# Performance work log

Hardware: AMD Instinct MI355X
Metric: run time of the kernel (lower is better)

## Reference

```python
import jax, jax.numpy as jnp
import numpy as np

THRESHOLD = 0.5
EPS = 1e-6

def setup_inputs() -> dict:
    key = jax.random.key(0)
    k1, k2, k3 = jax.random.split(key, 3)
    x = jax.random.normal(k1, (8192, 4096), dtype=jnp.float32)
    weight = jax.random.normal(k2, (16384, 4096), dtype=jnp.float32) * 0.02
    bias = jax.random.normal(k3, (16384,), dtype=jnp.float32) * 0.01
    return {"x": x, "weight": weight, "bias": bias}

def _quantize(weight):
    # abs-mean scale, ternarize to {-1,0,+1} with threshold, rescale
    scale = jnp.maximum(jnp.mean(jnp.abs(weight)), EPS)
    normalized = weight / scale
    ternary = jnp.sign(normalized) * (jnp.abs(normalized) > THRESHOLD).astype(weight.dtype)
    return ternary * scale

def reference(x, weight, bias):
    weight_q = _quantize(weight)
    # F.linear: x @ W^T + b
    return jnp.einsum('ti,oi->to', x, weight_q) + bias
```

## Files before the change

### kernel.cpp

```cpp
#include <hip/hip_runtime.h>
#include <hip/hip_bf16.h>

#define GLOBAL_AS __attribute__((address_space(1)))
#define LDS_AS    __attribute__((address_space(3)))

typedef __attribute__((ext_vector_type(8))) __bf16 bf16x8;
typedef __attribute__((ext_vector_type(4))) float  f32x4;

static constexpr int M = 8192;
static constexpr int N = 16384;
static constexpr int K = 4096;
static constexpr float W_EPS = 1e-6f;
#define INV_WCOUNT (1.0f / 67108864.0f)

__global__ void absum_kernel(const float4* __restrict__ w, float* __restrict__ out) {
  const int total = (N * K) / 4;
  int idx = blockIdx.x * blockDim.x + threadIdx.x;
  int stride = gridDim.x * blockDim.x;
  float s = 0.0f;
  for (int i = idx; i < total; i += stride) {
    float4 v = w[i];
    s += fabsf(v.x) + fabsf(v.y) + fabsf(v.z) + fabsf(v.w);
  }
  #pragma unroll
  for (int off = 32; off > 0; off >>= 1) s += __shfl_down(s, off, 64);
  __shared__ float red[4];
  const int lane = threadIdx.x & 63, wv = threadIdx.x >> 6;
  if (lane == 0) red[wv] = s;
  __syncthreads();
  if (threadIdx.x == 0) atomicAdd(out, red[0] + red[1] + red[2] + red[3]);
}

__global__ void quant_kernel(const float4* __restrict__ w, ushort4* __restrict__ wq,
                             const float* __restrict__ wsum) {
  const float s   = fmaxf(wsum[0] * INV_WCOUNT, W_EPS);
  const float thr = 0.5f * s;
  const int total = (N * K) / 4;
  int idx = blockIdx.x * blockDim.x + threadIdx.x;
  int stride = gridDim.x * blockDim.x;
  for (int i = idx; i < total; i += stride) {
    float4 v = w[i];
    ushort4 q;
    q.x = v.x > thr ? 0x3F80u : (v.x < -thr ? 0xBF80u : 0u);
    q.y = v.y > thr ? 0x3F80u : (v.y < -thr ? 0xBF80u : 0u);
    q.z = v.z > thr ? 0x3F80u : (v.z < -thr ? 0xBF80u : 0u);
    q.w = v.w > thr ? 0x3F80u : (v.w < -thr ? 0xBF80u : 0u);
    wq[i] = q;
  }
}

__device__ __forceinline__ unsigned short f2bf(float f) {
  unsigned int b = __float_as_uint(f);
  b += 0x7FFFu + ((b >> 16) & 1u);
  return (unsigned short)(b >> 16);
}

__global__ void castx_kernel(const float4* __restrict__ x, ushort4* __restrict__ xb) {
  const int total = (M * K) / 4;
  int idx = blockIdx.x * blockDim.x + threadIdx.x;
  int stride = gridDim.x * blockDim.x;
  for (int i = idx; i < total; i += stride) {
    float4 v = x[i];
    ushort4 q;
    q.x = f2bf(v.x); q.y = f2bf(v.y); q.z = f2bf(v.z); q.w = f2bf(v.w);
    xb[i] = q;
  }
}

#define STAGE(gp, ldsbase, tt, h) do {                                               \
    char* _l = (ldsbase) + ((tt) & 1) * 32768 + (h) * 16384 + wv * 1024;             \
    __builtin_amdgcn_global_load_lds((const GLOBAL_AS void*)(gp[h][0] + (size_t)(tt) * 64), \
                                     (LDS_AS void*)_l, 16, 0, 0);                    \
    __builtin_amdgcn_global_load_lds((const GLOBAL_AS void*)(gp[h][1] + (size_t)(tt) * 64), \
                                     (LDS_AS void*)(_l + 8192), 16, 0, 0);           \
  } while (0)

#define DSA(ih, bb) do {                                                             \
    _Pragma("unroll")                                                                \
    for (int i = 0; i < 4; ++i) {                                                    \
      Af[ih][i][0] = *(const bf16x8*)(paA0 + (bb) * 32768 + ((ih) * 64 + i * 16) * 128); \
      Af[ih][i][1] = *(const bf16x8*)(paA1 + (bb) * 32768 + ((ih) * 64 + i * 16) * 128); \
    }                                                                                \
  } while (0)

#define DSB(jh, bb) do {                                                             \
    _Pragma("unroll")                                                                \
    for (int j = 0; j < 2; ++j) {                                                    \
      Bf[jh][j][0] = *(const bf16x8*)(pbB0 + (bb) * 32768 + ((jh) * 32 + j * 16) * 128); \
      Bf[jh][j][1] = *(const bf16x8*)(pbB1 + (bb) * 32768 + ((jh) * 32 + j * 16) * 128); \
    }                                                                                \
  } while (0)

#define MFMAQ(ih, jh) do {                                                           \
    _Pragma("unroll")                                                                \
    for (int kk = 0; kk < 2; ++kk)                                                   \
      _Pragma("unroll")                                                              \
      for (int i = 0; i < 4; ++i)                                                    \
        _Pragma("unroll")                                                            \
        for (int j = 0; j < 2; ++j)                                                  \
          acc[(ih) * 4 + i][(jh) * 2 + j] = __builtin_amdgcn_mfma_f32_16x16x32_bf16( \
              Af[ih][i][kk], Bf[jh][j][kk], acc[(ih) * 4 + i][(jh) * 2 + j], 0, 0, 0); \
  } while (0)

__global__ __launch_bounds__(512, 2) void gemm_kernel(
    const __hip_bfloat16* __restrict__ A,
    const __hip_bfloat16* __restrict__ B,
    const float* __restrict__ bias,
    const float* __restrict__ wsum,
    float* __restrict__ out) {
  extern __shared__ char smem[];
  char* ldsA = smem;
  char* ldsB = smem + 65536;

  const int tid  = threadIdx.x;
  const int lane = tid & 63;
  const int wv   = tid >> 6;
  const int wm   = wv >> 2;
  const int wn   = wv & 3;
  const int tn   = blockIdx.x;
  const int tm   = blockIdx.y;

  const int srow = tid >> 3;
  const int sce  = ((((tid & 7) << 4) ^ ((srow & 7) << 4)) >> 1);
  const __hip_bfloat16* gA[2][2];
  const __hip_bfloat16* gB[2][2];
  #pragma unroll
  for (int h = 0; h < 2; ++h)
    #pragma unroll
    for (int c = 0; c < 2; ++c) {
      gA[h][c] = A + (size_t)(tm * 256 + h * 128 + c * 64 + srow) * K + sce;
      gB[h][c] = B + (size_t)(tn * 256 + h * 128 + c * 64 + srow) * K + sce;
    }

  const int arow = wm * 128 + (lane & 15);
  const int brow = wn * 64  + (lane & 15);
  const int xorv = (lane & 7) << 4;
  const int ac0  = (((lane >> 4) << 4) + 0)  ^ xorv;
  const int ac1  = (((lane >> 4) << 4) + 64) ^ xorv;
  const char* paA0 = ldsA + arow * 128 + ac0;
  const char* paA1 = ldsA + arow * 128 + ac1;
  const char* pbB0 = ldsB + brow * 128 + ac0;
  const char* pbB1 = ldsB + brow * 128 + ac1;

  const f32x4 zero = {0.f, 0.f, 0.f, 0.f};
  f32x4 acc[8][4];
  #pragma unroll
  for (int i = 0; i < 8; ++i)
    #pragma unroll
    for (int j = 0; j < 4; ++j) acc[i][j] = zero;

  bf16x8 Af[2][4][2];
  bf16x8 Bf[2][2][2];

  STAGE(gA, ldsA, 0, 0); STAGE(gA, ldsA, 0, 1);
  STAGE(gB, ldsB, 0, 0); STAGE(gB, ldsB, 0, 1);
  STAGE(gA, ldsA, 1, 0); STAGE(gA, ldsA, 1, 1);
  asm volatile("s_waitcnt vmcnt(4)" ::: "memory");
  __builtin_amdgcn_s_barrier();

  for (int t = 0; t < 64; ++t) {
    const int bb = t & 1;
    DSA(0, bb); DSB(0, bb);
    if (t + 1 < 64) STAGE(gB, ldsB, t + 1, 0);
    __builtin_amdgcn_s_barrier();
    asm volatile("s_waitcnt lgkmcnt(0)" ::: "memory");
    __builtin_amdgcn_sched_barrier(0);
    __builtin_amdgcn_s_setprio(1);
    MFMAQ(0, 0);
    __builtin_amdgcn_s_setprio(0);
    __builtin_amdgcn_s_barrier();
    DSA(1, bb);
    if (t + 1 < 64) STAGE(gB, ldsB, t + 1, 1);
    __builtin_amdgcn_s_barrier();
    asm volatile("s_waitcnt lgkmcnt(0)" ::: "memory");
    __builtin_amdgcn_sched_barrier(0);
    __builtin_amdgcn_s_setprio(1);
    MFMAQ(1, 0);
    __builtin_amdgcn_s_setprio(0);
    __builtin_amdgcn_s_barrier();
    DSB(1, bb);
    if (t + 2 < 64) STAGE(gA, ldsA, t + 2, 0);
    __builtin_amdgcn_s_barrier();
    asm volatile("s_waitcnt lgkmcnt(0)" ::: "memory");
    __builtin_amdgcn_sched_barrier(0);
    __builtin_amdgcn_s_setprio(1);
    MFMAQ(1, 1);
    __builtin_amdgcn_s_setprio(0);
    __builtin_amdgcn_s_barrier();
    if (t + 2 < 64) STAGE(gA, ldsA, t + 2, 1);
    __builtin_amdgcn_s_barrier();
    __builtin_amdgcn_s_setprio(1);
    MFMAQ(0, 1);
    __builtin_amdgcn_s_setprio(0);
    if (t < 62) asm volatile("s_waitcnt vmcnt(4)" ::: "memory");
    else        asm volatile("s_waitcnt vmcnt(0)" ::: "memory");
    __builtin_amdgcn_s_barrier();
  }

  const float s  = fmaxf(wsum[0] * INV_WCOUNT, W_EPS);
  const int   n0 = tn * 256 + wn * 64 + (lane & 15);
  const int   m0 = tm * 256 + wm * 128 + ((lane >> 4) << 2);
  float bj[4];
  #pragma unroll
  for (int j = 0; j < 4; ++j) bj[j] = bias[n0 + j * 16];
  #pragma unroll
  for (int i = 0; i < 8; ++i) {
    #pragma unroll
    for (int r = 0; r < 4; ++r) {
      float* orow = out + (size_t)(m0 + i * 16 + r) * N + n0;
      #pragma unroll
      for (int j = 0; j < 4; ++j)
        orow[j * 16] = acc[i][j][r] * s + bj[j];
    }
  }
}

extern "C" void kernel_launch(void* const* d_in, const int* in_sizes, int n_in,
                              void* d_out, int out_size, void* d_ws, size_t ws_size,
                              hipStream_t stream) {
  const float* x    = (const float*)d_in[0];
  const float* w    = (const float*)d_in[1];
  const float* bias = (const float*)d_in[2];
  float* out = (float*)d_out;

  char* ws = (char*)d_ws;
  float* wsum = (float*)ws;
  __hip_bfloat16* Wq = (__hip_bfloat16*)(ws + 256);
  __hip_bfloat16* Xb = (__hip_bfloat16*)(ws + 256 + (size_t)N * K * 2);

  static bool attr_set = false;
  if (!attr_set) {
    hipFuncSetAttribute((const void*)gemm_kernel,
                        hipFuncAttributeMaxDynamicSharedMemorySize, 131072);
    attr_set = true;
  }

  hipMemsetAsync(wsum, 0, sizeof(float), stream);
  absum_kernel<<<2048, 256, 0, stream>>>((const float4*)w, wsum);
  quant_kernel<<<8192, 256, 0, stream>>>((const float4*)w, (ushort4*)Wq, wsum);
  castx_kernel<<<4096, 256, 0, stream>>>((const float4*)x, (ushort4*)Xb);
  dim3 grid(N / 256, M / 256);
  gemm_kernel<<<grid, 512, 131072, stream>>>(Xb, Wq, bias, wsum, out);
}
```

Before: 1.602 ms.

## Fuse quant and cast prep kernels and deepen GEMM B-tile prefetch

Merges the weight ternarization and the x-to-bf16 cast into one launch that splits work by block index and writes 16-byte vectors, removing a kernel launch and widening stores. In the GEMM main loop, the B half-tile for step t+2 is now issued one phase earlier, the vmcnt wait is relaxed from 4 to 6, and the loop is unrolled by two with explicit tail iterations. The intent is to hide more global-to-LDS latency behind MFMA work, at the cost of tighter LDS buffer-reuse ordering that must stay correct across the barriers.

```diff
diff --git a/kernel.cpp b/kernel.cpp
--- a/kernel.cpp
+++ b/kernel.cpp
@@ -6,6 +6,7 @@
 
 typedef __attribute__((ext_vector_type(8))) __bf16 bf16x8;
 typedef __attribute__((ext_vector_type(4))) float  f32x4;
+typedef __attribute__((ext_vector_type(8))) unsigned short ushort8_t;
 
 static constexpr int M = 8192;
 static constexpr int N = 16384;
@@ -31,39 +32,44 @@
   if (threadIdx.x == 0) atomicAdd(out, red[0] + red[1] + red[2] + red[3]);
 }
 
-__global__ void quant_kernel(const float4* __restrict__ w, ushort4* __restrict__ wq,
-                             const float* __restrict__ wsum) {
-  const float s   = fmaxf(wsum[0] * INV_WCOUNT, W_EPS);
-  const float thr = 0.5f * s;
-  const int total = (N * K) / 4;
-  int idx = blockIdx.x * blockDim.x + threadIdx.x;
-  int stride = gridDim.x * blockDim.x;
-  for (int i = idx; i < total; i += stride) {
-    float4 v = w[i];
-    ushort4 q;
-    q.x = v.x > thr ? 0x3F80u : (v.x < -thr ? 0xBF80u : 0u);
-    q.y = v.y > thr ? 0x3F80u : (v.y < -thr ? 0xBF80u : 0u);
-    q.z = v.z > thr ? 0x3F80u : (v.z < -thr ? 0xBF80u : 0u);
-    q.w = v.w > thr ? 0x3F80u : (v.w < -thr ? 0xBF80u : 0u);
-    wq[i] = q;
-  }
-}
-
 __device__ __forceinline__ unsigned short f2bf(float f) {
   unsigned int b = __float_as_uint(f);
   b += 0x7FFFu + ((b >> 16) & 1u);
   return (unsigned short)(b >> 16);
 }
 
-__global__ void castx_kernel(const float4* __restrict__ x, ushort4* __restrict__ xb) {
-  const int total = (M * K) / 4;
-  int idx = blockIdx.x * blockDim.x + threadIdx.x;
-  int stride = gridDim.x * blockDim.x;
-  for (int i = idx; i < total; i += stride) {
-    float4 v = x[i];
-    ushort4 q;
-    q.x = f2bf(v.x); q.y = f2bf(v.y); q.z = f2bf(v.z); q.w = f2bf(v.w);
-    xb[i] = q;
+__device__ __forceinline__ unsigned short tern(float v, float thr) {
+  return v > thr ? 0x3F80u : (v < -thr ? 0xBF80u : 0u);
+}
+
+__global__ void prep_kernel(const float4* __restrict__ w, ushort8_t* __restrict__ wq,
+                            const float4* __restrict__ x, ushort8_t* __restrict__ xb,
+                            const float* __restrict__ wsum) {
+  const int b = blockIdx.x;
+  if (b < 8192) {
+    const float s   = fmaxf(wsum[0] * INV_WCOUNT, W_EPS);
+    const float thr = 0.5f * s;
+    const int total = (N * K) / 8;
+    int idx = b * 256 + threadIdx.x;
+    const int stride = 8192 * 256;
+    for (int i = idx; i < total; i += stride) {
+      float4 v0 = w[2 * i], v1 = w[2 * i + 1];
+      ushort8_t q;
+      q[0] = tern(v0.x, thr); q[1] = tern(v0.y, thr); q[2] = tern(v0.z, thr); q[3] = tern(v0.w, thr);
+      q[4] = tern(v1.x, thr); q[5] = tern(v1.y, thr); q[6] = tern(v1.z, thr); q[7] = tern(v1.w, thr);
+      wq[i] = q;
+    }
+  } else {
+    const int total = (M * K) / 8;
+    int idx = (b - 8192) * 256 + threadIdx.x;
+    const int stride = 4096 * 256;
+    for (int i = idx; i < total; i += stride) {
+      float4 v0 = x[2 * i], v1 = x[2 * i + 1];
+      ushort8_t q;
+      q[0] = f2bf(v0.x); q[1] = f2bf(v0.y); q[2] = f2bf(v0.z); q[3] = f2bf(v0.w);
+      q[4] = f2bf(v1.x); q[5] = f2bf(v1.y); q[6] = f2bf(v1.z); q[7] = f2bf(v1.w);
+      xb[i] = q;
+    }
   }
 }
 
@@ -102,6 +108,40 @@
               Af[ih][i][kk], Bf[jh][j][kk], acc[(ih) * 4 + i][(jh) * 2 + j], 0, 0, 0); \
   } while (0)
 
+#define LGKM0 do {                                                                   \
+    asm volatile("s_waitcnt lgkmcnt(0)" ::: "memory");                               \
+    __builtin_amdgcn_sched_barrier(0);                                               \
+  } while (0)
+
+#define PH_BAR __builtin_amdgcn_s_barrier()
+
+#define TILEBODY(t, bb, doS1, doS3, doS4, VMN) do {                                  \
+                                                   \
+    DSA(0, bb); DSB(0, bb);                                                          \
+    if (doS1) STAGE(gB, ldsB, (t) + 1, 1);                                           \
+    asm volatile("s_waitcnt lgkmcnt(8)" ::: "memory");                               \
+    PH_BAR; LGKM0;                                                                   \
+    __builtin_amdgcn_s_setprio(1); MFMAQ(0, 0); __builtin_amdgcn_s_setprio(0);       \
+    PH_BAR;                                                                          \
+                                                    \
+    DSA(1, bb);                                                                      \
+    PH_BAR; LGKM0;                                                                   \
+    __builtin_amdgcn_s_setprio(1); MFMAQ(1, 0); __builtin_amdgcn_s_setprio(0);       \
+    PH_BAR;                                                                          \
+                                \
+    DSB(1, bb);                                                                      \
+    if (doS3) STAGE(gA, ldsA, (t) + 2, 0);                                           \
+    PH_BAR; LGKM0;                                                                   \
+    __builtin_amdgcn_s_setprio(1); MFMAQ(1, 1); __builtin_amdgcn_s_setprio(0);       \
+    PH_BAR;                                                                          \
+                                \
+    if (doS4) { STAGE(gA, ldsA, (t) + 2, 1); STAGE(gB, ldsB, (t) + 2, 0); }          \
+    PH_BAR;                                                                          \
+    __builtin_amdgcn_s_setprio(1); MFMAQ(0, 1); __builtin_amdgcn_s_setprio(0);       \
+    asm volatile("s_waitcnt vmcnt(" #VMN ")" ::: "memory");                          \
+    PH_BAR;                                                                          \
+  } while (0)
+
 __global__ __launch_bounds__(512, 2) void gemm_kernel(
     const __hip_bfloat16* __restrict__ A,
     const __hip_bfloat16* __restrict__ B,
@@ -155,47 +195,16 @@
   STAGE(gA, ldsA, 0, 0); STAGE(gA, ldsA, 0, 1);
   STAGE(gB, ldsB, 0, 0); STAGE(gB, ldsB, 0, 1);
   STAGE(gA, ldsA, 1, 0); STAGE(gA, ldsA, 1, 1);
-  asm volatile("s_waitcnt vmcnt(4)" ::: "memory");
+  STAGE(gB, ldsB, 1, 0);
+  asm volatile("s_waitcnt vmcnt(6)" ::: "memory");
   __builtin_amdgcn_s_barrier();
 
-  for (int t = 0; t < 64; ++t) {
-    const int bb = t & 1;
-    DSA(0, bb); DSB(0, bb);
-    if (t + 1 < 64) STAGE(gB, ldsB, t + 1, 0);
-    __builtin_amdgcn_s_barrier();
-    asm volatile("s_waitcnt lgkmcnt(0)" ::: "memory");
-    __builtin_amdgcn_sched_barrier(0);
-    __builtin_amdgcn_s_setprio(1);
-    MFMAQ(0, 0);
-    __builtin_amdgcn_s_setprio(0);
-    __builtin_amdgcn_s_barrier();
-    DSA(1, bb);
-    if (t + 1 < 64) STAGE(gB, ldsB, t + 1, 1);
-    __builtin_amdgcn_s_barrier();
-    asm volatile("s_waitcnt lgkmcnt(0)" ::: "memory");
-    __builtin_amdgcn_sched_barrier(0);
-    __builtin_amdgcn_s_setprio(1);
-    MFMAQ(1, 0);
-    __builtin_amdgcn_s_setprio(0);
-    __builtin_amdgcn_s_barrier();
-    DSB(1, bb);
-    if (t + 2 < 64) STAGE(gA, ldsA, t + 2, 0);
-    __builtin_amdgcn_s_barrier();
-    asm volatile("s_waitcnt lgkmcnt(0)" ::: "memory");
-    __builtin_amdgcn_sched_barrier(0);
-    __builtin_amdgcn_s_setprio(1);
-    MFMAQ(1, 1);
-    __builtin_amdgcn_s_setprio(0);
-    __builtin_amdgcn_s_barrier();
-    if (t + 2 < 64) STAGE(gA, ldsA, t + 2, 1);
-    __builtin_amdgcn_s_barrier();
-    __builtin_amdgcn_s_setprio(1);
-    MFMAQ(0, 1);
-    __builtin_amdgcn_s_setprio(0);
-    if (t < 62) asm volatile("s_waitcnt vmcnt(4)" ::: "memory");
-    else        asm volatile("s_waitcnt vmcnt(0)" ::: "memory");
-    __builtin_amdgcn_s_barrier();
-  }
+  for (int t = 0; t < 62; t += 2) {
+    TILEBODY(t,     0, 1, 1, 1, 6);
+    TILEBODY(t + 1, 1, 1, 1, 1, 6);
+  }
+  TILEBODY(62, 0, 1, 0, 0, 0);
+  TILEBODY(63, 1, 0, 0, 0, 0);
 
   const float s  = fmaxf(wsum[0] * INV_WCOUNT, W_EPS);
   const int   n0 = tn * 256 + wn * 64 + (lane & 15);
@@ -237,8 +246,8 @@
 
   hipMemsetAsync(wsum, 0, sizeof(float), stream);
   absum_kernel<<<2048, 256, 0, stream>>>((const float4*)w, wsum);
-  quant_kernel<<<8192, 256, 0, stream>>>((const float4*)w, (ushort4*)Wq, wsum);
-  castx_kernel<<<4096, 256, 0, stream>>>((const float4*)x, (ushort4*)Xb);
+  prep_kernel<<<12288, 256, 0, stream>>>((const float4*)w, (ushort8_t*)Wq,
+                                         (const float4*)x, (ushort8_t*)Xb, wsum);
   dim3 grid(N / 256, M / 256);
   gemm_kernel<<<grid, 512, 131072, stream>>>(Xb, Wq, bias, wsum, out);
 }
```

Measured after the change: 1.628 ms. About the same (+1.6%).
